# Performance work log

Measured on AMD Instinct MI355X. Metric: run time of the kernel, lower is better.

Reference implementation:

```python
import jax, jax.numpy as jnp
import numpy as np

NUM_EXPERTS = 8
TOP_K = 2
HIDDEN = 1024
INTER = 3584
BATCH = 2
SEQ = 2048
TOKENS = BATCH * SEQ


def setup_inputs() -> dict:
    key = jax.random.key(0)
    k_h, k_l, k_w1, k_w2, k_w3 = jax.random.split(key, 5)
    hidden_states = jax.random.normal(k_h, (TOKENS, HIDDEN), dtype=jnp.float32)
    # Router: top-2 over softmaxed logits, renormalized (standard Mixtral routing)
    logits = jax.random.normal(k_l, (TOKENS, NUM_EXPERTS), dtype=jnp.float32)
    probs = jax.nn.softmax(logits, axis=-1)
    routing_weights, selected = jax.lax.top_k(probs, TOP_K)  # [T, K], [T, K]
    routing_weights = routing_weights / jnp.sum(routing_weights, axis=-1, keepdims=True)
    # expert_mask: [num_experts, top_k, tokens]
    expert_mask = jax.nn.one_hot(selected, NUM_EXPERTS, dtype=jnp.int32).transpose(2, 1, 0)
    scale = 0.02
    w1 = jax.random.normal(k_w1, (NUM_EXPERTS, HIDDEN, INTER), dtype=jnp.float32) * scale
    w2 = jax.random.normal(k_w2, (NUM_EXPERTS, INTER, HIDDEN), dtype=jnp.float32) * scale
    w3 = jax.random.normal(k_w3, (NUM_EXPERTS, HIDDEN, INTER), dtype=jnp.float32) * scale
    return {
        "expert_mask": expert_mask,
        "hidden_states": hidden_states,
        "routing_weights": routing_weights,
        "w1": w1,
        "w2": w2,
        "w3": w3,
        "batch_size": BATCH,
        "sequence_length": SEQ,
        "hidden_dim": HIDDEN,
    }


def reference(expert_mask, hidden_states, routing_weights, w1, w2, w3,
              batch_size, sequence_length, hidden_dim):
    num_experts = w1.shape[0]
    tokens = batch_size * sequence_length
    # Extra row at the end absorbs writes from fill_value=-1 padding (as in source).
    final = jnp.zeros((tokens + 1, hidden_dim), dtype=hidden_states.dtype)
    for e in range(num_experts):
        # idx: which top-k slot; top_x: which token. Padded with -1.
        idx, top_x = jnp.nonzero(expert_mask[e], size=sequence_length, fill_value=-1)
        cur = hidden_states[top_x]  # [S, H]
        h = (jax.nn.silu(cur @ w1[e]) * (cur @ w3[e])) @ w2[e]  # SwiGLU MLP
        h = h * routing_weights[top_x, idx, None]
        final = final.at[top_x].set(h + final[top_x])
    final = final[:-1]
    return final.reshape(batch_size, sequence_length, hidden_dim)
```

## Files before the change

kernel.cpp:

```cpp
#include <hip/hip_runtime.h>
#include <hip/hip_bf16.h>
#include <cstdint>
#include <cstddef>

#define NEXP  8
#define NTOK  4096
#define HID   1024
#define INTER 3584
#define CAP   2048

#define BM  128
#define BN  128
#define BK  32

typedef __attribute__((ext_vector_type(4))) float floatx4;
typedef __attribute__((ext_vector_type(8))) short shortx8;
typedef unsigned short u16;

__device__ __forceinline__ u16 f2bf(float f) {
    union { float f; unsigned u; } v; v.f = f;
    unsigned r = v.u + 0x7fffu + ((v.u >> 16) & 1u);
    return (u16)(r >> 16);
}

__device__ __forceinline__ shortx8 pack8(const float* v) {
    shortx8 r;
#pragma unroll
    for (int i = 0; i < 8; ++i) r[i] = (short)f2bf(v[i]);
    return r;
}

__device__ __forceinline__ unsigned cvt_pk_bf16(float a, float b) {
    unsigned r;
    asm("v_cvt_pk_bf16_f32 %0, %1, %2" : "=v"(r) : "v"(a), "v"(b));
    return r;
}

__device__ __forceinline__ void async_ld16(const void* g, void* l) {
    __builtin_amdgcn_global_load_lds(
        (const __attribute__((address_space(1))) unsigned int*)g,
        (__attribute__((address_space(3))) unsigned int*)l, 16, 0, 0);
}

__device__ __forceinline__ void wait_vm0_barrier() {
    asm volatile("s_waitcnt vmcnt(0)" ::: "memory");
    __builtin_amdgcn_s_barrier();
    __builtin_amdgcn_sched_barrier(0);
}

__global__ void route_kernel(const int* __restrict__ mask, const float* __restrict__ rw,
                             int* __restrict__ cnt, int* __restrict__ list,
                             float* __restrict__ wgt) {
    int t = blockIdx.x * blockDim.x + threadIdx.x;
    if (t >= NTOK) return;
#pragma unroll
    for (int e = 0; e < NEXP; ++e) {
#pragma unroll
        for (int k = 0; k < 2; ++k) {
            if (mask[(e * 2 + k) * NTOK + t] != 0) {
                int pos = atomicAdd(&cnt[e], 1);
                if (pos < CAP) {
                    list[e * CAP + pos] = t;
                    wgt[e * CAP + pos] = rw[t * 2 + k];
                }
            }
        }
    }
}

__global__ void xcvt_kernel(const float* __restrict__ X, u16* __restrict__ Xb) {
    const int i = (blockIdx.x * 256 + threadIdx.x) * 8;
    float4 a = *(const float4*)&X[i];
    float4 b = *(const float4*)&X[i + 4];
    float v[8] = {a.x, a.y, a.z, a.w, b.x, b.y, b.z, b.w};
    *(shortx8*)&Xb[i] = pack8(v);
}

__global__ void transpose_cvt_all_kernel(const float* __restrict__ w1,
                                         const float* __restrict__ w2,
                                         const float* __restrict__ w3,
                                         u16* __restrict__ W1b, u16* __restrict__ W2b,
                                         u16* __restrict__ W3b) {
    const int wsel = blockIdx.z;
    const int e    = blockIdx.y;
    const float* src; u16* dst; int K, N, nx;
    if (wsel == 0)      { src = w1; dst = W1b; K = HID;   N = INTER; nx = INTER / 64; }
    else if (wsel == 1) { src = w3; dst = W3b; K = HID;   N = INTER; nx = INTER / 64; }
    else                { src = w2; dst = W2b; K = INTER; N = HID;   nx = HID / 64;   }
    src += (size_t)e * K * N;
    dst += (size_t)e * K * N;
    const int tile = blockIdx.x;
    const int n0 = (tile % nx) * 64;
    const int k0 = (tile / nx) * 64;

    __shared__ unsigned ldsT[64 * 34];
    const int tid = threadIdx.x;
    {
        const int np = tid & 15;
        const int kp = tid >> 4;
        const float* sp = src + (size_t)(k0 + kp * 4) * N + n0 + np * 4;
        float4 r0 = *(const float4*)sp;
        float4 r1 = *(const float4*)(sp + (size_t)N);
        float4 r2 = *(const float4*)(sp + 2 * (size_t)N);
        float4 r3 = *(const float4*)(sp + 3 * (size_t)N);
        const float c0[4] = {r0.x, r0.y, r0.z, r0.w};
        const float c1[4] = {r1.x, r1.y, r1.z, r1.w};
        const float c2[4] = {r2.x, r2.y, r2.z, r2.w};
        const float c3[4] = {r3.x, r3.y, r3.z, r3.w};
#pragma unroll
        for (int j = 0; j < 4; ++j) {
            const int n = np * 4 + j;
            uint2 w;
            w.x = cvt_pk_bf16(c0[j], c1[j]);
            w.y = cvt_pk_bf16(c2[j], c3[j]);
            *(uint2*)&ldsT[n * 34 + kp * 2] = w;
        }
    }
    __syncthreads();
    {
        const int n = tid >> 2;
        const int q = tid & 3;
        unsigned r[8];
#pragma unroll
        for (int i = 0; i < 4; ++i) {
            uint2 v = *(const uint2*)&ldsT[n * 34 + (q * 4 + i) * 2];
            r[i * 2] = v.x; r[i * 2 + 1] = v.y;
        }
        u16* dp = dst + (size_t)(n0 + n) * K + k0 + q * 16;
        *(uint4*)&dp[0] = *(const uint4*)&r[0];
        *(uint4*)&dp[8] = *(const uint4*)&r[4];
    }
}

__global__ __launch_bounds__(256, 2)
void gemm1_kernel(const u16* __restrict__ Xb, const u16* __restrict__ W1b,
                  const u16* __restrict__ W3b, const int* __restrict__ cnt,
                  const int* __restrict__ list, const float* __restrict__ wgt,
                  u16* __restrict__ H) {
    const int e  = blockIdx.z;
    const int ce = min(cnt[e], CAP);
    const int m0 = blockIdx.y * BM;
    if (m0 >= ce) return;
    const int n0 = blockIdx.x * BN;

    __shared__ u16 sm[2 * 3 * BM * BK];

    const int tid  = threadIdx.x;
    const int lane = tid & 63;
    const int wave = tid >> 6;

    const int srow0 = wave * 32 + (lane >> 2);
    const int srow1 = srow0 + 16;
    const int s0   = (srow0 >> 1) & 3;
    const int scol = ((lane & 3) ^ s0) * 8;
    const int lo0 = wave * 1024 + lane * 8;
    const int lo1 = lo0 + 512;

    const int t0 = list[e * CAP + min(m0 + srow0, ce - 1)];
    const int t1 = list[e * CAP + min(m0 + srow1, ce - 1)];
    const u16* ap0  = Xb + (size_t)t0 * HID + scol;
    const u16* ap1  = Xb + (size_t)t1 * HID + scol;
    const u16* b1p0 = W1b + ((size_t)e * INTER + n0 + srow0) * HID + scol;
    const u16* b1p1 = b1p0 + (size_t)16 * HID;
    const u16* b3p0 = W3b + ((size_t)e * INTER + n0 + srow0) * HID + scol;
    const u16* b3p1 = b3p0 + (size_t)16 * HID;

    const int fl = lane & 15, fq = lane >> 4;
    const int fqs = (fq ^ ((fl >> 1) & 3)) * 8;
    const int wm  = (wave >> 1) * 64;
    const int wnn = (wave & 1) * 64;

    auto stage = [&](int b, int kk) {
        u16* base = sm + b * (3 * BM * BK);
        async_ld16(ap0  + kk, base + lo0);
        async_ld16(ap1  + kk, base + lo1);
        async_ld16(b1p0 + kk, base + BM * BK + lo0);
        async_ld16(b1p1 + kk, base + BM * BK + lo1);
        async_ld16(b3p0 + kk, base + 2 * BM * BK + lo0);
        async_ld16(b3p1 + kk, base + 2 * BM * BK + lo1);
    };

    floatx4 acc1[4][4], acc3[4][4];
#pragma unroll
    for (int i = 0; i < 4; ++i)
#pragma unroll
        for (int j = 0; j < 4; ++j)
#pragma unroll
            for (int r = 0; r < 4; ++r) { acc1[i][j][r] = 0.f; acc3[i][j][r] = 0.f; }

    const int NT = HID / BK;
    stage(0, 0);
    wait_vm0_barrier();

    int cur = 0;
    for (int t = 0; t < NT; ++t) {
        if (t + 1 < NT) stage(cur ^ 1, (t + 1) * BK);

        const u16* bA  = sm + cur * (3 * BM * BK);
        const u16* bB1 = bA + BM * BK;
        const u16* bB3 = bA + 2 * BM * BK;

        shortx8 af[4], b1f[4], b3f[4];
#pragma unroll
        for (int i = 0; i < 4; ++i)
            af[i] = *(const shortx8*)&bA[(wm + i * 16 + fl) * BK + fqs];
#pragma unroll
        for (int j = 0; j < 4; ++j) {
            b1f[j] = *(const shortx8*)&bB1[(wnn + j * 16 + fl) * BK + fqs];
            b3f[j] = *(const shortx8*)&bB3[(wnn + j * 16 + fl) * BK + fqs];
        }
#pragma unroll
        for (int i = 0; i < 4; ++i)
#pragma unroll
            for (int j = 0; j < 4; ++j) {
                acc1[i][j] = __builtin_amdgcn_mfma_f32_16x16x32_bf16(af[i], b1f[j], acc1[i][j], 0, 0, 0);
                acc3[i][j] = __builtin_amdgcn_mfma_f32_16x16x32_bf16(af[i], b3f[j], acc3[i][j], 0, 0, 0);
            }

        wait_vm0_barrier();
        cur ^= 1;
    }

#pragma unroll
    for (int i = 0; i < 4; ++i) {
        const int rowb = m0 + wm + i * 16 + fq * 4;
#pragma unroll
        for (int r = 0; r < 4; ++r) {
            const int row = rowb + r;
            const bool valid = row < ce;
            const float rwv = valid ? wgt[e * CAP + row] : 0.f;
            u16* hp = H + (size_t)(e * CAP + (valid ? row : 0)) * INTER;
#pragma unroll
            for (int j = 0; j < 4; ++j) {
                const int col = n0 + wnn + j * 16 + fl;
                float h1 = acc1[i][j][r];
                float h3 = acc3[i][j][r];
                float sv = h1 / (1.f + __expf(-h1)) * h3 * rwv;
                if (valid) hp[col] = f2bf(sv);
            }
        }
    }
}

__global__ __launch_bounds__(256, 2)
void gemm2_kernel(const u16* __restrict__ H, const u16* __restrict__ W2b,
                  const int* __restrict__ cnt, const int* __restrict__ list,
                  float* __restrict__ out) {
    const int e  = blockIdx.z;
    const int ce = min(cnt[e], CAP);
    const int m0 = blockIdx.y * BM;
    if (m0 >= ce) return;
    const int n0 = blockIdx.x * BN;

    __shared__ u16 sm[2 * 2 * BM * BK];

    const int tid  = threadIdx.x;
    const int lane = tid & 63;
    const int wave = tid >> 6;

    const int srow0 = wave * 32 + (lane >> 2);
    const int s0   = (srow0 >> 1) & 3;
    const int scol = ((lane & 3) ^ s0) * 8;
    const int lo0 = wave * 1024 + lane * 8;
    const int lo1 = lo0 + 512;

    const u16* ap0 = H + (size_t)(e * CAP + m0 + srow0) * INTER + scol;
    const u16* ap1 = ap0 + (size_t)16 * INTER;
    const u16* bp0 = W2b + ((size_t)e * HID + n0 + srow0) * INTER + scol;
    const u16* bp1 = bp0 + (size_t)16 * INTER;

    const int fl = lane & 15, fq = lane >> 4;
    const int fqs = (fq ^ ((fl >> 1) & 3)) * 8;
    const int wm  = (wave >> 1) * 64;
    const int wnn = (wave & 1) * 64;

    auto stage = [&](int b, int kk) {
        u16* base = sm + b * (2 * BM * BK);
        async_ld16(ap0 + kk, base + lo0);
        async_ld16(ap1 + kk, base + lo1);
        async_ld16(bp0 + kk, base + BM * BK + lo0);
        async_ld16(bp1 + kk, base + BM * BK + lo1);
    };

    floatx4 acc[4][4];
#pragma unroll
    for (int i = 0; i < 4; ++i)
#pragma unroll
        for (int j = 0; j < 4; ++j)
#pragma unroll
            for (int r = 0; r < 4; ++r) acc[i][j][r] = 0.f;

    const int NT = INTER / BK;
    stage(0, 0);
    wait_vm0_barrier();

    int cur = 0;
    for (int t = 0; t < NT; ++t) {
        if (t + 1 < NT) stage(cur ^ 1, (t + 1) * BK);

        const u16* bA = sm + cur * (2 * BM * BK);
        const u16* bB = bA + BM * BK;

        shortx8 af[4], bf[4];
#pragma unroll
        for (int i = 0; i < 4; ++i)
            af[i] = *(const shortx8*)&bA[(wm + i * 16 + fl) * BK + fqs];
#pragma unroll
        for (int j = 0; j < 4; ++j)
            bf[j] = *(const shortx8*)&bB[(wnn + j * 16 + fl) * BK + fqs];
#pragma unroll
        for (int i = 0; i < 4; ++i)
#pragma unroll
            for (int j = 0; j < 4; ++j)
                acc[i][j] = __builtin_amdgcn_mfma_f32_16x16x32_bf16(af[i], bf[j], acc[i][j], 0, 0, 0);

        wait_vm0_barrier();
        cur ^= 1;
    }

#pragma unroll
    for (int i = 0; i < 4; ++i) {
        const int rowb = m0 + wm + i * 16 + fq * 4;
#pragma unroll
        for (int r = 0; r < 4; ++r) {
            const int row = rowb + r;
            const bool valid = row < ce;
            const int tok = valid ? list[e * CAP + row] : 0;
            float* op = out + (size_t)tok * HID;
#pragma unroll
            for (int j = 0; j < 4; ++j) {
                const int col = n0 + wnn + j * 16 + fl;
                if (valid) atomicAdd(&op[col], acc[i][j][r]);
            }
        }
    }
}

extern "C" void kernel_launch(void* const* d_in, const int* in_sizes, int n_in,
                              void* d_out, int out_size, void* d_ws, size_t ws_size,
                              hipStream_t stream) {
    const int*   mask = (const int*)  d_in[0];
    const float* X    = (const float*)d_in[1];
    const float* rw   = (const float*)d_in[2];
    const float* w1   = (const float*)d_in[3];
    const float* w2   = (const float*)d_in[4];
    const float* w3   = (const float*)d_in[5];
    float* out = (float*)d_out;

    char* ws = (char*)d_ws;
    size_t off = 0;
    int*   cnt  = (int*)(ws + off);  off += 256;
    int*   list = (int*)(ws + off);  off += (size_t)NEXP * CAP * 4;
    float* wgt  = (float*)(ws + off); off += (size_t)NEXP * CAP * 4;
    u16*   Xb   = (u16*)(ws + off);  off += (size_t)NTOK * HID * 2;
    u16*   W1b  = (u16*)(ws + off);  off += (size_t)NEXP * HID * INTER * 2;
    u16*   W3b  = (u16*)(ws + off);  off += (size_t)NEXP * HID * INTER * 2;
    u16*   W2b  = (u16*)(ws + off);  off += (size_t)NEXP * HID * INTER * 2;
    u16*   H    = (u16*)(ws + off);  off += (size_t)NEXP * CAP * INTER * 2;

    hipMemsetAsync(cnt, 0, 256, stream);
    hipMemsetAsync(d_out, 0, (size_t)out_size * sizeof(float), stream);

    route_kernel<<<dim3((NTOK + 255) / 256), dim3(256), 0, stream>>>(mask, rw, cnt, list, wgt);
    xcvt_kernel<<<dim3(NTOK * HID / (256 * 8)), dim3(256), 0, stream>>>(X, Xb);
    transpose_cvt_all_kernel<<<dim3((HID / 64) * (INTER / 64), NEXP, 3), dim3(256), 0, stream>>>(
        w1, w2, w3, W1b, W2b, W3b);

    gemm1_kernel<<<dim3(INTER / BN, CAP / BM, NEXP), dim3(256), 0, stream>>>(Xb, W1b, W3b, cnt, list, wgt, H);
    gemm2_kernel<<<dim3(HID / BN, CAP / BM, NEXP), dim3(256), 0, stream>>>(H, W2b, cnt, list, out);
}
```

Measured before the change: 694.1 us.

## Triple-buffer LDS in both expert GEMMs with partial vmcnt waits

Both GEMM kernels switch from a double-buffered K loop that waits for all outstanding loads to a three-stage ring. Loads run two tiles ahead, and each iteration waits only until the current tile has landed, using a partial vmcnt count. The aim is to hide global-to-LDS latency behind the MFMA work. In exchange, gemm1 needs 72KB of dynamic shared memory and gemm2 needs 48KB, which may cut occupancy below the two blocks per CU set in launch bounds.

```diff
diff --git a/kernel.cpp b/kernel.cpp
--- a/kernel.cpp
+++ b/kernel.cpp
@@ -17,6 +17,8 @@
 typedef __attribute__((ext_vector_type(8))) short shortx8;
 typedef unsigned short u16;
 
+#define WAITVM(N) asm volatile("s_waitcnt vmcnt(" #N ")" ::: "memory")
+
 __device__ __forceinline__ u16 f2bf(float f) {
     union { float f; unsigned u; } v; v.f = f;
     unsigned r = v.u + 0x7fffu + ((v.u >> 16) & 1u);
@@ -40,12 +42,6 @@
     __builtin_amdgcn_global_load_lds(
         (const __attribute__((address_space(1))) unsigned int*)g,
         (__attribute__((address_space(3))) unsigned int*)l, 16, 0, 0);
-}
-
-__device__ __forceinline__ void wait_vm0_barrier() {
-    asm volatile("s_waitcnt vmcnt(0)" ::: "memory");
-    __builtin_amdgcn_s_barrier();
-    __builtin_amdgcn_sched_barrier(0);
 }
 
 __global__ void route_kernel(const int* __restrict__ mask, const float* __restrict__ rw,
@@ -137,13 +133,12 @@
                   const u16* __restrict__ W3b, const int* __restrict__ cnt,
                   const int* __restrict__ list, const float* __restrict__ wgt,
                   u16* __restrict__ H) {
+    extern __shared__ u16 sm[];
     const int e  = blockIdx.z;
     const int ce = min(cnt[e], CAP);
     const int m0 = blockIdx.y * BM;
     if (m0 >= ce) return;
     const int n0 = blockIdx.x * BN;
-
-    __shared__ u16 sm[2 * 3 * BM * BK];
 
     const int tid  = threadIdx.x;
     const int lane = tid & 63;
@@ -188,18 +183,9 @@
 #pragma unroll
             for (int r = 0; r < 4; ++r) { acc1[i][j][r] = 0.f; acc3[i][j][r] = 0.f; }
 
-    const int NT = HID / BK;
-    stage(0, 0);
-    wait_vm0_barrier();
-
-    int cur = 0;
-    for (int t = 0; t < NT; ++t) {
-        if (t + 1 < NT) stage(cur ^ 1, (t + 1) * BK);
-
-        const u16* bA  = sm + cur * (3 * BM * BK);
+    auto compute = [&](const u16* bA) {
         const u16* bB1 = bA + BM * BK;
         const u16* bB3 = bA + 2 * BM * BK;
-
         shortx8 af[4], b1f[4], b3f[4];
 #pragma unroll
         for (int i = 0; i < 4; ++i)
@@ -216,10 +202,28 @@
                 acc1[i][j] = __builtin_amdgcn_mfma_f32_16x16x32_bf16(af[i], b1f[j], acc1[i][j], 0, 0, 0);
                 acc3[i][j] = __builtin_amdgcn_mfma_f32_16x16x32_bf16(af[i], b3f[j], acc3[i][j], 0, 0, 0);
             }
-
-        wait_vm0_barrier();
-        cur ^= 1;
-    }
+    };
+
+    const int NT = HID / BK;
+    stage(0, 0);
+    stage(1, BK);
+
+    int ct = 0;
+    for (int t = 0; t < NT - 1; ++t) {
+        WAITVM(6);
+        __builtin_amdgcn_s_barrier();
+        __builtin_amdgcn_sched_barrier(0);
+        if (t + 2 < NT) {
+            int sb = ct + 2; if (sb >= 3) sb -= 3;
+            stage(sb, (t + 2) * BK);
+        }
+        compute(sm + ct * (3 * BM * BK));
+        ct = (ct == 2) ? 0 : ct + 1;
+    }
+    WAITVM(0);
+    __builtin_amdgcn_s_barrier();
+    __builtin_amdgcn_sched_barrier(0);
+    compute(sm + ct * (3 * BM * BK));
 
 #pragma unroll
     for (int i = 0; i < 4; ++i) {
@@ -252,7 +256,7 @@
     if (m0 >= ce) return;
     const int n0 = blockIdx.x * BN;
 
-    __shared__ u16 sm[2 * 2 * BM * BK];
+    __shared__ u16 sm[3 * 2 * BM * BK];
 
     const int tid  = threadIdx.x;
     const int lane = tid & 63;
@@ -290,33 +294,42 @@
 #pragma unroll
             for (int r = 0; r < 4; ++r) acc[i][j][r] = 0.f;
 
+    auto compute = [&](const u16* bA) {
+        const u16* bB = bA + BM * BK;
+        shortx8 af[4], bf[4];
+#pragma unroll
+        for (int i = 0; i < 4; ++i)
+            af[i] = *(const shortx8*)&bA[(wm + i * 16 + fl) * BK + fqs];
+#pragma unroll
+        for (int j = 0; j < 4; ++j)
+            bf[j] = *(const shortx8*)&bB[(wnn + j * 16 + fl) * BK + fqs];
+#pragma unroll
+        for (int i = 0; i < 4; ++i)
+#pragma unroll
+            for (int j = 0; j < 4; ++j)
+                acc[i][j] = __builtin_amdgcn_mfma_f32_16x16x32_bf16(af[i], bf[j], acc[i][j], 0, 0, 0);
+    };
+
     const int NT = INTER / BK;
     stage(0, 0);
-    wait_vm0_barrier();
-
-    int cur = 0;
-    for (int t = 0; t < NT; ++t) {
-        if (t + 1 < NT) stage(cur ^ 1, (t + 1) * BK);
-
-        const u16* bA = sm + cur * (2 * BM * BK);
-        const u16* bB = bA + BM * BK;
-
-        shortx8 af[4], bf[4];
-#pragma unroll
-        for (int i = 0; i < 4; ++i)
-            af[i] = *(const shortx8*)&bA[(wm + i * 16 + fl) * BK + fqs];
-#pragma unroll
-        for (int j = 0; j < 4; ++j)
-            bf[j] = *(const shortx8*)&bB[(wnn + j * 16 + fl) * BK + fqs];
-#pragma unroll
-        for (int i = 0; i < 4; ++i)
-#pragma unroll
-            for (int j = 0; j < 4; ++j)
-                acc[i][j] = __builtin_amdgcn_mfma_f32_16x16x32_bf16(af[i], bf[j], acc[i][j], 0, 0, 0);
-
-        wait_vm0_barrier();
-        cur ^= 1;
-    }
+    stage(1, BK);
+
+    int ct = 0;
+    for (int t = 0; t < NT - 1; ++t) {
+        WAITVM(4);
+        __builtin_amdgcn_s_barrier();
+        __builtin_amdgcn_sched_barrier(0);
+        if (t + 2 < NT) {
+            int sb = ct + 2; if (sb >= 3) sb -= 3;
+            stage(sb, (t + 2) * BK);
+        }
+        compute(sm + ct * (2 * BM * BK));
+        ct = (ct == 2) ? 0 : ct + 1;
+    }
+    WAITVM(0);
+    __builtin_amdgcn_s_barrier();
+    __builtin_amdgcn_sched_barrier(0);
+    compute(sm + ct * (2 * BM * BK));
 
 #pragma unroll
     for (int i = 0; i < 4; ++i) {
@@ -358,6 +371,13 @@
     u16*   W2b  = (u16*)(ws + off);  off += (size_t)NEXP * HID * INTER * 2;
     u16*   H    = (u16*)(ws + off);  off += (size_t)NEXP * CAP * INTER * 2;
 
+    static bool attr_done = false;
+    if (!attr_done) {
+        (void)hipFuncSetAttribute((const void*)gemm1_kernel,
+                                  hipFuncAttributeMaxDynamicSharedMemorySize, 73728);
+        attr_done = true;
+    }
+
     hipMemsetAsync(cnt, 0, 256, stream);
     hipMemsetAsync(d_out, 0, (size_t)out_size * sizeof(float), stream);
 
@@ -366,6 +386,6 @@
     transpose_cvt_all_kernel<<<dim3((HID / 64) * (INTER / 64), NEXP, 3), dim3(256), 0, stream>>>(
         w1, w2, w3, W1b, W2b, W3b);
 
-    gemm1_kernel<<<dim3(INTER / BN, CAP / BM, NEXP), dim3(256), 0, stream>>>(Xb, W1b, W3b, cnt, list, wgt, H);
+    gemm1_kernel<<<dim3(INTER / BN, CAP / BM, NEXP), dim3(256), 73728, stream>>>(Xb, W1b, W3b, cnt, list, wgt, H);
     gemm2_kernel<<<dim3(HID / BN, CAP / BM, NEXP), dim3(256), 0, stream>>>(H, W2b, cnt, list, out);
 }
```

Measured after the change: 661.1 us. -4.8%, faster.
